# Optimization experiments

Hardware: AMD Instinct MI355X
Metric: run time of the kernel (lower is better)

The kernel has to match this reference:

```python
import jax, jax.numpy as jnp
import numpy as np

EPS = 1e-5

def _rmsnorm(x):
    # BitLinear applies a (non-learnable) RMSNorm to activations before quantization
    return x * jax.lax.rsqrt(jnp.mean(x * x, axis=-1, keepdims=True) + EPS)

def _activation_quant(x):
    # per-token absmax int8 quantization, dequantized back to float
    scale = 127.0 / jnp.clip(jnp.max(jnp.abs(x), axis=-1, keepdims=True), EPS, None)
    return jnp.clip(jnp.round(x * scale), -128, 127) / scale

def _weight_quant(w):
    # absmean ternary {-1,0,1} quantization, dequantized back to float
    scale = 1.0 / jnp.clip(jnp.mean(jnp.abs(w)), EPS, None)
    return jnp.clip(jnp.round(w * scale), -1, 1) / scale

def _bitlinear(x, w):
    xn = _rmsnorm(x)
    # straight-through estimators (identity grads through quantizers)
    xq = xn + jax.lax.stop_gradient(_activation_quant(xn) - xn)
    wq = w + jax.lax.stop_gradient(_weight_quant(w) - w)
    return jnp.einsum('bsd,hd->bsh', xq, wq)

def setup_inputs() -> dict:
    key = jax.random.key(0)
    k1, k2, k3, k4 = jax.random.split(key, 4)
    B, S, D, H = 4, 2048, 4096, 11008
    return {
        'x': jax.random.normal(k1, (B, S, D), dtype=jnp.float32),
        'w_gate': jax.random.normal(k2, (H, D), dtype=jnp.float32) * 0.02,
        'w_up': jax.random.normal(k3, (H, D), dtype=jnp.float32) * 0.02,
        'w_down': jax.random.normal(k4, (D, H), dtype=jnp.float32) * 0.02,
    }

def reference(x, w_gate, w_up, w_down):
    h = jax.nn.silu(_bitlinear(x, w_gate)) * _bitlinear(x, w_up)
    return _bitlinear(h, w_down)
```

## Files before the change

### kernel.cpp

```cpp
#include <hip/hip_runtime.h>
#include <hip/hip_bf16.h>
#include <cstdint>

#define EPS 1e-5

typedef __attribute__((ext_vector_type(4))) int int32x4;

__device__ __forceinline__ void gload(const char* g, char* l) {
  __builtin_amdgcn_global_load_lds(
      (const __attribute__((address_space(1))) unsigned int*)g,
      (__attribute__((address_space(3))) unsigned int*)l, 16, 0, 0);
}

__device__ inline float np_leaf_abs(const float* __restrict__ a, int n) {
  float r[8];
  #pragma unroll
  for (int j = 0; j < 8; j++) r[j] = fabsf(a[j]);
  for (int i = 8; i < n; i += 8) {
    #pragma unroll
    for (int j = 0; j < 8; j++) r[j] += fabsf(a[i + j]);
  }
  return ((r[0] + r[1]) + (r[2] + r[3])) + ((r[4] + r[5]) + (r[6] + r[7]));
}

__global__ __launch_bounds__(256) void np_blocksums(
    const float* __restrict__ w, float* __restrict__ bs) {
  int b = blockIdx.x * 256 + threadIdx.x;
  const float* a = w + (long)b * 344;
  float s0 = np_leaf_abs(a, 80);
  float s1 = np_leaf_abs(a + 80, 88);
  float s2 = np_leaf_abs(a + 168, 88);
  float s3 = np_leaf_abs(a + 256, 88);
  bs[b] = (s0 + s1) + (s2 + s3);
}

__global__ __launch_bounds__(256) void np_tree_partial(
    const float* __restrict__ bs, float* __restrict__ part) {
  __shared__ float sh[256];
  int t = threadIdx.x;
  const float* a = bs + (long)blockIdx.x * 512;
  sh[t] = a[2 * t] + a[2 * t + 1];
  __syncthreads();
  for (int n = 128; n >= 1; n >>= 1) {
    float x = 0.f;
    if (t < n) x = sh[2 * t] + sh[2 * t + 1];
    __syncthreads();
    if (t < n) sh[t] = x;
    __syncthreads();
  }
  if (t == 0) part[blockIdx.x] = sh[0];
}

__global__ __launch_bounds__(128) void np_tree_final(
    const float* __restrict__ part, float* __restrict__ out) {
  __shared__ float sh[128];
  int t = threadIdx.x;
  sh[t] = part[2 * t] + part[2 * t + 1];
  __syncthreads();
  for (int n = 64; n >= 1; n >>= 1) {
    float x = 0.f;
    if (t < n) x = sh[2 * t] + sh[2 * t + 1];
    __syncthreads();
    if (t < n) sh[t] = x;
    __syncthreads();
  }
  if (t == 0) out[0] = sh[0] / 45088768.0f;
}

__global__ __launch_bounds__(256) void quant_w(
    const float* __restrict__ w, const float* __restrict__ mean_ptr,
    char* __restrict__ q, long n4) {
  float scale = 1.0f / fmaxf(*mean_ptr, 1e-5f);
  long i = (long)blockIdx.x * blockDim.x + threadIdx.x;
  long stride = (long)gridDim.x * blockDim.x;
  const float4* w4 = (const float4*)w;
  char4* q4 = (char4*)q;
  for (; i < n4; i += stride) {
    float4 v = w4[i];
    char4 c;
    c.x = (char)(int)fminf(1.f, fmaxf(-1.f, rintf(v.x * scale)));
    c.y = (char)(int)fminf(1.f, fmaxf(-1.f, rintf(v.y * scale)));
    c.z = (char)(int)fminf(1.f, fmaxf(-1.f, rintf(v.z * scale)));
    c.w = (char)(int)fminf(1.f, fmaxf(-1.f, rintf(v.w * scale)));
    q4[i] = c;
  }
}

#define CORR_MAX 1024
#define WIN 1e-6f

__global__ __launch_bounds__(256) void quant_w_down(
    const float* __restrict__ w, const float* __restrict__ mean_ptr,
    char* __restrict__ q, int* __restrict__ cnt,
    int* __restrict__ ck, float* __restrict__ cv) {
  float scale = 1.0f / fmaxf(*mean_ptr, 1e-5f);
  long i0 = ((long)blockIdx.x * blockDim.x + threadIdx.x) * 4;
  long stride = (long)gridDim.x * blockDim.x * 4;
  for (long i = i0; i < 4096L * 11008L; i += stride) {
    char4 c;
    #pragma unroll
    for (int j = 0; j < 4; j++) {
      float t = w[i + j] * scale;
      float qv = fminf(1.f, fmaxf(-1.f, rintf(t)));
      if (fabsf(fabsf(t) - 0.5f) < WIN) {
        qv = 0.f;
        int idx = atomicAdd(cnt, 1);
        if (idx < CORR_MAX) {
          ck[idx] = (int)(i + j);
          cv[idx] = t > 0.f ? 0.5f : -0.5f;
        }
      }
      ((char*)&c)[j] = (char)(int)qv;
    }
    *(char4*)(q + i) = c;
  }
}

__global__ void zero_cnt(int* cnt) { *cnt = 0; }

__global__ __launch_bounds__(64) void apply_corr(
    const int* __restrict__ cnt, const int* __restrict__ ck,
    const float* __restrict__ cv, const char* __restrict__ qh,
    const float* __restrict__ fh, const float* __restrict__ meanw,
    float* __restrict__ out) {
  int r = blockIdx.x * 64 + threadIdx.x;
  float fwd = fmaxf(meanw[2], 1e-5f);
  int n = *cnt; if (n > CORR_MAX) n = CORR_MAX;
  float fr = fh[r] * fwd;
  for (int i = 0; i < n; i++) {
    int flat = ck[i];
    int nn = flat / 11008, kk = flat % 11008;
    float qv = (float)qh[(long)r * 11008 + kk];
    out[(long)r * 4096 + nn] += cv[i] * qv * fr;
  }
}

__device__ inline void block_reduce_sum_max_d(double& s, float& m) {
  #pragma unroll
  for (int off = 1; off < 64; off <<= 1) {
    s += __shfl_xor(s, off, 64);
    m = fmaxf(m, __shfl_xor(m, off, 64));
  }
  __shared__ double ssh[4];
  __shared__ float msh[4];
  int wv = threadIdx.x >> 6;
  if ((threadIdx.x & 63) == 0) { ssh[wv] = s; msh[wv] = m; }
  __syncthreads();
  s = (ssh[0] + ssh[1]) + (ssh[2] + ssh[3]);
  m = fmaxf(fmaxf(msh[0], msh[1]), fmaxf(msh[2], msh[3]));
}

__device__ inline char quant1d(float x, double rn, double s) {
  double t = (double)x * rn;
  double q = rint(t * s);
  q = fmin(127.0, fmax(-128.0, q));
  return (char)(int)q;
}

__global__ __launch_bounds__(256) void act_quant_x(
    const float* __restrict__ x, char* __restrict__ qx, float* __restrict__ fx) {
  const int row = blockIdx.x;
  const float4* xr = (const float4*)(x + (long)row * 4096);
  float4 v[4];
  double ss = 0.0;
  float am = 0.f;
  #pragma unroll
  for (int i = 0; i < 4; i++) {
    v[i] = xr[i * 256 + threadIdx.x];
    ss += ((double)v[i].x * v[i].x + (double)v[i].y * v[i].y) +
          ((double)v[i].z * v[i].z + (double)v[i].w * v[i].w);
    am = fmaxf(am, fmaxf(fmaxf(fabsf(v[i].x), fabsf(v[i].y)),
                         fmaxf(fabsf(v[i].z), fabsf(v[i].w))));
  }
  block_reduce_sum_max_d(ss, am);
  double rn = 1.0 / sqrt(ss / 4096.0 + EPS);
  double den = fmax((double)am * rn, EPS);
  double s = 127.0 / den;
  if (threadIdx.x == 0) fx[row] = (float)(den / 127.0);
  char4* qr = (char4*)(qx + (long)row * 4096);
  #pragma unroll
  for (int i = 0; i < 4; i++) {
    char4 c;
    c.x = quant1d(v[i].x, rn, s);
    c.y = quant1d(v[i].y, rn, s);
    c.z = quant1d(v[i].z, rn, s);
    c.w = quant1d(v[i].w, rn, s);
    qr[i * 256 + threadIdx.x] = c;
  }
}

__global__ __launch_bounds__(256) void act_quant_h(
    const float* __restrict__ h, char* __restrict__ qh, float* __restrict__ fh) {
  const long row = blockIdx.x;
  const float4* hr = (const float4*)(h + row * 11008);
  double ss = 0.0;
  float am = 0.f;
  for (int i = threadIdx.x; i < 2752; i += 256) {
    float4 v = hr[i];
    ss += ((double)v.x * v.x + (double)v.y * v.y) +
          ((double)v.z * v.z + (double)v.w * v.w);
    am = fmaxf(am, fmaxf(fmaxf(fabsf(v.x), fabsf(v.y)),
                         fmaxf(fabsf(v.z), fabsf(v.w))));
  }
  block_reduce_sum_max_d(ss, am);
  double rn = 1.0 / sqrt(ss / 11008.0 + EPS);
  double den = fmax((double)am * rn, EPS);
  double s = 127.0 / den;
  if (threadIdx.x == 0) fh[row] = (float)(den / 127.0);
  char4* qr = (char4*)(qh + row * 11008);
  for (int i = threadIdx.x; i < 2752; i += 256) {
    float4 v = hr[i];
    char4 c;
    c.x = quant1d(v.x, rn, s);
    c.y = quant1d(v.y, rn, s);
    c.z = quant1d(v.z, rn, s);
    c.w = quant1d(v.w, rn, s);
    qr[i] = c;
  }
}


__global__ __launch_bounds__(256, 2) void gemm_gateup(
    const char* __restrict__ qx, const char* __restrict__ qwg, const char* __restrict__ qwu,
    const float* __restrict__ meanw, const float* __restrict__ fx, float* __restrict__ h) {
  __shared__ __align__(16) char As[3][8192];
  __shared__ __align__(16) char Bgs[3][8192];
  __shared__ __align__(16) char Bus[3][8192];
  const int t = threadIdx.x;
  const int lane = t & 63;
  const int wv = t >> 6;
  const int bid = blockIdx.x;
  const int swz = (bid & 7) * 688 + (bid >> 3);
  const int m0 = (swz & 63) * 128;
  const int n0 = (swz >> 6) * 128;
  const int wm = (wv >> 1) * 64;
  const int wn = (wv & 1) * 64;

  const int rowin = lane >> 2;
  const int gcol = (((lane & 3) - ((lane >> 3) & 3)) & 3) * 16;
  const int slot = ((((lane >> 4) + ((lane >> 1) & 3)) & 3) << 4);
  const int lrow = (lane & 15) * 64;

  const char* gA = qx  + (long)(m0 + wv * 32 + rowin) * 4096 + gcol;
  const char* gG = qwg + (long)(n0 + wv * 32 + rowin) * 4096 + gcol;
  const char* gU = qwu + (long)(n0 + wv * 32 + rowin) * 4096 + gcol;
  const long R16 = 16L * 4096;

  int32x4 accg[4][4] = {};
  int32x4 accu[4][4] = {};

  #define STAGE_GU(pb, k0)                                 \
    do {                                                   \
      gload(gA + (k0),       &As [pb][wv * 2048]);         \
      gload(gA + (k0) + R16, &As [pb][wv * 2048 + 1024]);  \
      gload(gG + (k0),       &Bgs[pb][wv * 2048]);         \
      gload(gG + (k0) + R16, &Bgs[pb][wv * 2048 + 1024]);  \
      gload(gU + (k0),       &Bus[pb][wv * 2048]);         \
      gload(gU + (k0) + R16, &Bus[pb][wv * 2048 + 1024]);  \
    } while (0)

  STAGE_GU(0, 0);
  STAGE_GU(1, 64);
  asm volatile("s_waitcnt vmcnt(6)" ::: "memory");
  __builtin_amdgcn_s_barrier();

  for (int ks = 0; ks < 64; ++ks) {
    const int pb = ks % 3;
    const char* ab = &As [pb][0] + wm * 64 + lrow + slot;
    const char* gb = &Bgs[pb][0] + wn * 64 + lrow + slot;
    const char* ub = &Bus[pb][0] + wn * 64 + lrow + slot;
    int32x4 a[4], bg[4], bu[4];
    #pragma unroll
    for (int m = 0; m < 4; m++) a[m] = *(const int32x4*)(ab + m * 1024);
    #pragma unroll
    for (int n = 0; n < 4; n++) bg[n] = *(const int32x4*)(gb + n * 1024);
    #pragma unroll
    for (int n = 0; n < 4; n++) bu[n] = *(const int32x4*)(ub + n * 1024);
    if (ks + 2 < 64) STAGE_GU((ks + 2) % 3, (ks + 2) * 64);
    __builtin_amdgcn_s_setprio(1);
    #pragma unroll
    for (int n = 0; n < 4; n++) {
      #pragma unroll
      for (int m = 0; m < 4; m++) {
        accg[m][n] = __builtin_amdgcn_mfma_i32_16x16x64_i8(a[m], bg[n], accg[m][n], 0, 0, 0);
        accu[m][n] = __builtin_amdgcn_mfma_i32_16x16x64_i8(a[m], bu[n], accu[m][n], 0, 0, 0);
      }
    }
    __builtin_amdgcn_s_setprio(0);
    if (ks < 62)      asm volatile("s_waitcnt vmcnt(6)" ::: "memory");
    else if (ks < 63) asm volatile("s_waitcnt vmcnt(0)" ::: "memory");
    if (ks < 63) __builtin_amdgcn_s_barrier();
  }
  #undef STAGE_GU

  float fwg = fmaxf(meanw[0], 1e-5f);
  float fwu = fmaxf(meanw[1], 1e-5f);
  const int rgrp = lane >> 4;
  const int cidx = lane & 15;
  #pragma unroll
  for (int m = 0; m < 4; m++) {
    #pragma unroll
    for (int r = 0; r < 4; r++) {
      int grow = m0 + wm + m * 16 + rgrp * 4 + r;
      float fxr = fx[grow];
      float sg = fxr * fwg, su = fxr * fwu;
      #pragma unroll
      for (int n = 0; n < 4; n++) {
        float g = (float)accg[m][n][r] * sg;
        float u = (float)accu[m][n][r] * su;
        float hv = g / (1.f + expf(-g)) * u;
        h[(long)grow * 11008 + (n0 + wn + n * 16 + cidx)] = hv;
      }
    }
  }
}

__global__ __launch_bounds__(256, 3) void gemm_down(
    const char* __restrict__ qh, const char* __restrict__ qwd,
    const float* __restrict__ mean_wd, const float* __restrict__ fh,
    float* __restrict__ out) {
  __shared__ __align__(16) char As[3][8192];
  __shared__ __align__(16) char Bs[3][8192];
  const int t = threadIdx.x;
  const int lane = t & 63;
  const int wv = t >> 6;
  const int bid = blockIdx.x;
  const int swz = (bid & 7) * 256 + (bid >> 3);
  const int m0 = (swz & 63) * 128;
  const int n0 = (swz >> 6) * 128;
  const int wm = (wv >> 1) * 64;
  const int wn = (wv & 1) * 64;

  const int rowin = lane >> 2;
  const int gcol = (((lane & 3) - ((lane >> 3) & 3)) & 3) * 16;
  const int slot = ((((lane >> 4) + ((lane >> 1) & 3)) & 3) << 4);
  const int lrow = (lane & 15) * 64;

  const char* gA = qh  + (long)(m0 + wv * 32 + rowin) * 11008 + gcol;
  const char* gB = qwd + (long)(n0 + wv * 32 + rowin) * 11008 + gcol;
  const long R16 = 16L * 11008;

  int32x4 acc[4][4] = {};

  #define STAGE_DN(pb, k0)                                \
    do {                                                  \
      gload(gA + (k0),       &As[pb][wv * 2048]);         \
      gload(gA + (k0) + R16, &As[pb][wv * 2048 + 1024]);  \
      gload(gB + (k0),       &Bs[pb][wv * 2048]);         \
      gload(gB + (k0) + R16, &Bs[pb][wv * 2048 + 1024]);  \
    } while (0)

  STAGE_DN(0, 0);
  STAGE_DN(1, 64);
  asm volatile("s_waitcnt vmcnt(4)" ::: "memory");
  __builtin_amdgcn_s_barrier();

  for (int ks = 0; ks < 172; ++ks) {
    const int pb = ks % 3;
    const char* ab = &As[pb][0] + wm * 64 + lrow + slot;
    const char* bb = &Bs[pb][0] + wn * 64 + lrow + slot;
    int32x4 a[4], b[4];
    #pragma unroll
    for (int m = 0; m < 4; m++) a[m] = *(const int32x4*)(ab + m * 1024);
    #pragma unroll
    for (int n = 0; n < 4; n++) b[n] = *(const int32x4*)(bb + n * 1024);
    if (ks + 2 < 172) STAGE_DN((ks + 2) % 3, (ks + 2) * 64);
    __builtin_amdgcn_s_setprio(1);
    #pragma unroll
    for (int n = 0; n < 4; n++) {
      #pragma unroll
      for (int m = 0; m < 4; m++)
        acc[m][n] = __builtin_amdgcn_mfma_i32_16x16x64_i8(a[m], b[n], acc[m][n], 0, 0, 0);
    }
    __builtin_amdgcn_s_setprio(0);
    if (ks < 170)      asm volatile("s_waitcnt vmcnt(4)" ::: "memory");
    else if (ks < 171) asm volatile("s_waitcnt vmcnt(0)" ::: "memory");
    if (ks < 171) __builtin_amdgcn_s_barrier();
  }
  #undef STAGE_DN

  float fwd = fmaxf(mean_wd[0], 1e-5f);
  const int rgrp = lane >> 4;
  const int cidx = lane & 15;
  #pragma unroll
  for (int m = 0; m < 4; m++) {
    #pragma unroll
    for (int r = 0; r < 4; r++) {
      int grow = m0 + wm + m * 16 + rgrp * 4 + r;
      float f = fh[grow] * fwd;
      #pragma unroll
      for (int n = 0; n < 4; n++) {
        out[(long)grow * 4096 + (n0 + wn + n * 16 + cidx)] =
            (float)acc[m][n][r] * f;
      }
    }
  }
}

extern "C" void kernel_launch(void* const* d_in, const int* in_sizes, int n_in,
                              void* d_out, int out_size, void* d_ws, size_t ws_size,
                              hipStream_t stream) {
  const float* x      = (const float*)d_in[0];
  const float* w_gate = (const float*)d_in[1];
  const float* w_up   = (const float*)d_in[2];
  const float* w_down = (const float*)d_in[3];
  float* out = (float*)d_out;

  const long NW = 11008L * 4096L;
  const long NX = 8192L * 4096L;
  const long NH = 8192L * 11008L;

  char* ws  = (char*)d_ws;
  char* qwg = ws;
  char* qwu = qwg + NW;
  char* qwd = qwu + NW;
  char* qx  = qwd + NW;
  char* qh  = qx + NX;
  float* h  = (float*)(qh + NH);
  float* fx = h + NH;
  float* fh = fx + 8192;
  float* meanw = fh + 8192;
  float* bs    = meanw + 4;
  float* tmp   = bs + 131072;
  int*   ccnt  = (int*)(tmp + 65536);
  int*   ck    = ccnt + 4;
  float* cv    = (float*)(ck + CORR_MAX);

  zero_cnt<<<1, 1, 0, stream>>>(ccnt);

  np_blocksums<<<512, 256, 0, stream>>>(w_gate, bs);
  np_tree_partial<<<256, 256, 0, stream>>>(bs, tmp);
  np_tree_final<<<1, 128, 0, stream>>>(tmp, meanw + 0);
  np_blocksums<<<512, 256, 0, stream>>>(w_up, bs);
  np_tree_partial<<<256, 256, 0, stream>>>(bs, tmp);
  np_tree_final<<<1, 128, 0, stream>>>(tmp, meanw + 1);
  np_blocksums<<<512, 256, 0, stream>>>(w_down, bs);
  np_tree_partial<<<256, 256, 0, stream>>>(bs, tmp);
  np_tree_final<<<1, 128, 0, stream>>>(tmp, meanw + 2);

  quant_w<<<4096, 256, 0, stream>>>(w_gate, meanw + 0, qwg, NW / 4);
  quant_w<<<4096, 256, 0, stream>>>(w_up,   meanw + 1, qwu, NW / 4);
  quant_w_down<<<4096, 256, 0, stream>>>(w_down, meanw + 2, qwd, ccnt, ck, cv);

  act_quant_x<<<8192, 256, 0, stream>>>(x, qx, fx);

  gemm_gateup<<<5504, 256, 0, stream>>>(qx, qwg, qwu, meanw, fx, h);

  act_quant_h<<<8192, 256, 0, stream>>>(h, qh, fh);

  gemm_down<<<2048, 256, 0, stream>>>(qh, qwd, meanw + 2, fh, out);

  apply_corr<<<128, 64, 0, stream>>>(ccnt, ck, cv, qh, fh, meanw, out);
}
```

Measured before the change: 1.881 ms.

## Batch weight reductions, prefetch LDS fragments in GEMMs, widen down-proj tile

The three weight-mean reduction chains are merged into single launches covering all three matrices, and the gate and up quantization kernels are merged into one launch. act_quant_h now caches its row in shared memory so the second pass does not re-read global memory. Both GEMMs move to a deeper 3-stage prefetch with register double-buffering of the LDS fragments, and gemm_down widens its N tile to 256. These changes cut launch overhead and global re-reads and aim to overlap LDS reads with MFMA, at the cost of more registers and LDS, which may lower occupancy.

```diff
diff --git a/kernel.cpp b/kernel.cpp
--- a/kernel.cpp
+++ b/kernel.cpp
@@ -23,10 +23,13 @@
   return ((r[0] + r[1]) + (r[2] + r[3])) + ((r[4] + r[5]) + (r[6] + r[7]));
 }
 
-__global__ __launch_bounds__(256) void np_blocksums(
-    const float* __restrict__ w, float* __restrict__ bs) {
+__global__ __launch_bounds__(256) void np_blocksums3(
+    const float* __restrict__ w0, const float* __restrict__ w1,
+    const float* __restrict__ w2, float* __restrict__ bs) {
   int b = blockIdx.x * 256 + threadIdx.x;
-  const float* a = w + (long)b * 344;
+  const float* w = (b < 131072) ? w0 : (b < 262144 ? w1 : w2);
+  long lb = b & 131071;
+  const float* a = w + lb * 344;
   float s0 = np_leaf_abs(a, 80);
   float s1 = np_leaf_abs(a + 80, 88);
   float s2 = np_leaf_abs(a + 168, 88);
@@ -34,7 +37,7 @@
   bs[b] = (s0 + s1) + (s2 + s3);
 }
 
-__global__ __launch_bounds__(256) void np_tree_partial(
+__global__ __launch_bounds__(256) void np_tree_partial3(
     const float* __restrict__ bs, float* __restrict__ part) {
   __shared__ float sh[256];
   int t = threadIdx.x;
@@ -51,11 +54,12 @@
   if (t == 0) part[blockIdx.x] = sh[0];
 }
 
-__global__ __launch_bounds__(128) void np_tree_final(
-    const float* __restrict__ part, float* __restrict__ out) {
+__global__ __launch_bounds__(128) void np_tree_final3(
+    const float* __restrict__ part, float* __restrict__ meanw) {
   __shared__ float sh[128];
   int t = threadIdx.x;
-  sh[t] = part[2 * t] + part[2 * t + 1];
+  const float* p = part + blockIdx.x * 256;
+  sh[t] = p[2 * t] + p[2 * t + 1];
   __syncthreads();
   for (int n = 64; n >= 1; n >>= 1) {
     float x = 0.f;
@@ -64,15 +68,19 @@
     if (t < n) sh[t] = x;
     __syncthreads();
   }
-  if (t == 0) out[0] = sh[0] / 45088768.0f;
-}
-
-__global__ __launch_bounds__(256) void quant_w(
-    const float* __restrict__ w, const float* __restrict__ mean_ptr,
-    char* __restrict__ q, long n4) {
-  float scale = 1.0f / fmaxf(*mean_ptr, 1e-5f);
-  long i = (long)blockIdx.x * blockDim.x + threadIdx.x;
-  long stride = (long)gridDim.x * blockDim.x;
+  if (t == 0) meanw[blockIdx.x] = sh[0] / 45088768.0f;
+}
+
+__global__ __launch_bounds__(256) void quant_w_gu(
+    const float* __restrict__ wg, const float* __restrict__ wu,
+    const float* __restrict__ meanw, char* __restrict__ qg, char* __restrict__ qu,
+    long n4) {
+  int half = (blockIdx.x >= 4096);
+  const float* w = half ? wu : wg;
+  char* q = half ? qu : qg;
+  float scale = 1.0f / fmaxf(meanw[half], 1e-5f);
+  long i = (long)(blockIdx.x & 4095) * blockDim.x + threadIdx.x;
+  long stride = 4096L * blockDim.x;
   const float4* w4 = (const float4*)w;
   char4* q4 = (char4*)q;
   for (; i < n4; i += stride) {
@@ -93,7 +101,7 @@
     const float* __restrict__ w, const float* __restrict__ mean_ptr,
     char* __restrict__ q, int* __restrict__ cnt,
     int* __restrict__ ck, float* __restrict__ cv) {
-  float scale = 1.0f / fmaxf(*mean_ptr, 1e-5f);
+  float scale = 1.0f / fmaxf(mean_ptr[2], 1e-5f);
   long i0 = ((long)blockIdx.x * blockDim.x + threadIdx.x) * 4;
   long stride = (long)gridDim.x * blockDim.x * 4;
   for (long i = i0; i < 4096L * 11008L; i += stride) {
@@ -191,12 +199,14 @@
 
 __global__ __launch_bounds__(256) void act_quant_h(
     const float* __restrict__ h, char* __restrict__ qh, float* __restrict__ fh) {
+  __shared__ float4 hrow4[2752];
   const long row = blockIdx.x;
   const float4* hr = (const float4*)(h + row * 11008);
   double ss = 0.0;
   float am = 0.f;
   for (int i = threadIdx.x; i < 2752; i += 256) {
     float4 v = hr[i];
+    hrow4[i] = v;
     ss += ((double)v.x * v.x + (double)v.y * v.y) +
           ((double)v.z * v.z + (double)v.w * v.w);
     am = fmaxf(am, fmaxf(fmaxf(fabsf(v.x), fabsf(v.y)),
@@ -209,7 +219,7 @@
   if (threadIdx.x == 0) fh[row] = (float)(den / 127.0);
   char4* qr = (char4*)(qh + row * 11008);
   for (int i = threadIdx.x; i < 2752; i += 256) {
-    float4 v = hr[i];
+    float4 v = hrow4[i];
     char4 c;
     c.x = quant1d(v.x, rn, s);
     c.y = quant1d(v.y, rn, s);
@@ -238,8 +248,7 @@
 
   const int rowin = lane >> 2;
   const int gcol = (((lane & 3) - ((lane >> 3) & 3)) & 3) * 16;
-  const int slot = ((((lane >> 4) + ((lane >> 1) & 3)) & 3) << 4);
-  const int lrow = (lane & 15) * 64;
+  const int loff = (lane & 15) * 64 + ((((lane >> 4) + ((lane >> 1) & 3)) & 3) << 4);
 
   const char* gA = qx  + (long)(m0 + wv * 32 + rowin) * 4096 + gcol;
   const char* gG = qwg + (long)(n0 + wv * 32 + rowin) * 4096 + gcol;
@@ -248,50 +257,85 @@
 
   int32x4 accg[4][4] = {};
   int32x4 accu[4][4] = {};
-
-  #define STAGE_GU(pb, k0)                                 \
-    do {                                                   \
-      gload(gA + (k0),       &As [pb][wv * 2048]);         \
-      gload(gA + (k0) + R16, &As [pb][wv * 2048 + 1024]);  \
-      gload(gG + (k0),       &Bgs[pb][wv * 2048]);         \
-      gload(gG + (k0) + R16, &Bgs[pb][wv * 2048 + 1024]);  \
-      gload(gU + (k0),       &Bus[pb][wv * 2048]);         \
-      gload(gU + (k0) + R16, &Bus[pb][wv * 2048 + 1024]);  \
-    } while (0)
-
-  STAGE_GU(0, 0);
-  STAGE_GU(1, 64);
+  int32x4 a0[4], g0[4], u0[4], a1[4], g1[4], u1[4];
+
+  char *PA0 = &As[0][0], *PA1 = &As[1][0], *PA2 = &As[2][0];
+  char *PG0 = &Bgs[0][0], *PG1 = &Bgs[1][0], *PG2 = &Bgs[2][0];
+  char *PU0 = &Bus[0][0], *PU1 = &Bus[1][0], *PU2 = &Bus[2][0];
+
+  #define GU_STAGE(pa, pg, pu, k0)                          \
+    do {                                                    \
+      gload(gA + (k0),       (pa) + wv * 2048);             \
+      gload(gA + (k0) + R16, (pa) + wv * 2048 + 1024);      \
+      gload(gG + (k0),       (pg) + wv * 2048);             \
+      gload(gG + (k0) + R16, (pg) + wv * 2048 + 1024);      \
+      gload(gU + (k0),       (pu) + wv * 2048);             \
+      gload(gU + (k0) + R16, (pu) + wv * 2048 + 1024);      \
+    } while (0)
+
+  #define GU_READ(ar, gr, ur, pa, pg, pu)                          \
+    do {                                                           \
+      _Pragma("unroll")                                            \
+      for (int m = 0; m < 4; m++)                                  \
+        ar[m] = *(const int32x4*)((pa) + (wm + m * 16) * 64 + loff); \
+      _Pragma("unroll")                                            \
+      for (int n = 0; n < 4; n++) {                                \
+        gr[n] = *(const int32x4*)((pg) + (wn + n * 16) * 64 + loff); \
+        ur[n] = *(const int32x4*)((pu) + (wn + n * 16) * 64 + loff); \
+      }                                                            \
+    } while (0)
+
+  #define GU_MFMA(ar, gr, ur)                                                \
+    do {                                                                     \
+      __builtin_amdgcn_s_setprio(1);                                         \
+      _Pragma("unroll")                                                      \
+      for (int n = 0; n < 4; n++) {                                          \
+        _Pragma("unroll")                                                    \
+        for (int m = 0; m < 4; m++) {                                        \
+          accg[m][n] = __builtin_amdgcn_mfma_i32_16x16x64_i8(ar[m], gr[n], accg[m][n], 0, 0, 0); \
+          accu[m][n] = __builtin_amdgcn_mfma_i32_16x16x64_i8(ar[m], ur[n], accu[m][n], 0, 0, 0); \
+        }                                                                    \
+      }                                                                      \
+      __builtin_amdgcn_s_setprio(0);                                         \
+    } while (0)
+
+  #define GU_ROT()                                          \
+    do {                                                    \
+      char* tp;                                             \
+      tp = PA0; PA0 = PA1; PA1 = PA2; PA2 = tp;             \
+      tp = PG0; PG0 = PG1; PG1 = PG2; PG2 = tp;             \
+      tp = PU0; PU0 = PU1; PU1 = PU2; PU2 = tp;             \
+    } while (0)
+
+  #define GU_BODY(ks, Rc_a, Rc_g, Rc_u, Rn_a, Rn_g, Rn_u)          \
+    do {                                                           \
+      if ((ks) + 3 < 64) GU_STAGE(PA0, PG0, PU0, ((ks) + 3) * 64); \
+      if ((ks) + 1 < 64) GU_READ(Rn_a, Rn_g, Rn_u, PA1, PG1, PU1); \
+      GU_MFMA(Rc_a, Rc_g, Rc_u);                                   \
+      if ((ks) + 3 < 64) asm volatile("s_waitcnt vmcnt(6)" ::: "memory"); \
+      else               asm volatile("s_waitcnt vmcnt(0)" ::: "memory"); \
+      if ((ks) < 62) __builtin_amdgcn_s_barrier();                 \
+      GU_ROT();                                                    \
+    } while (0)
+
+  GU_STAGE(PA0, PG0, PU0, 0);
+  GU_STAGE(PA1, PG1, PU1, 64);
+  GU_STAGE(PA2, PG2, PU2, 128);
+  asm volatile("s_waitcnt vmcnt(12)" ::: "memory");
+  __builtin_amdgcn_s_barrier();
+  GU_READ(a0, g0, u0, PA0, PG0, PU0);
   asm volatile("s_waitcnt vmcnt(6)" ::: "memory");
   __builtin_amdgcn_s_barrier();
 
-  for (int ks = 0; ks < 64; ++ks) {
-    const int pb = ks % 3;
-    const char* ab = &As [pb][0] + wm * 64 + lrow + slot;
-    const char* gb = &Bgs[pb][0] + wn * 64 + lrow + slot;
-    const char* ub = &Bus[pb][0] + wn * 64 + lrow + slot;
-    int32x4 a[4], bg[4], bu[4];
-    #pragma unroll
-    for (int m = 0; m < 4; m++) a[m] = *(const int32x4*)(ab + m * 1024);
-    #pragma unroll
-    for (int n = 0; n < 4; n++) bg[n] = *(const int32x4*)(gb + n * 1024);
-    #pragma unroll
-    for (int n = 0; n < 4; n++) bu[n] = *(const int32x4*)(ub + n * 1024);
-    if (ks + 2 < 64) STAGE_GU((ks + 2) % 3, (ks + 2) * 64);
-    __builtin_amdgcn_s_setprio(1);
-    #pragma unroll
-    for (int n = 0; n < 4; n++) {
-      #pragma unroll
-      for (int m = 0; m < 4; m++) {
-        accg[m][n] = __builtin_amdgcn_mfma_i32_16x16x64_i8(a[m], bg[n], accg[m][n], 0, 0, 0);
-        accu[m][n] = __builtin_amdgcn_mfma_i32_16x16x64_i8(a[m], bu[n], accu[m][n], 0, 0, 0);
-      }
-    }
-    __builtin_amdgcn_s_setprio(0);
-    if (ks < 62)      asm volatile("s_waitcnt vmcnt(6)" ::: "memory");
-    else if (ks < 63) asm volatile("s_waitcnt vmcnt(0)" ::: "memory");
-    if (ks < 63) __builtin_amdgcn_s_barrier();
-  }
-  #undef STAGE_GU
+  for (int ks = 0; ks < 64; ks += 2) {
+    GU_BODY(ks,     a0, g0, u0, a1, g1, u1);
+    GU_BODY(ks + 1, a1, g1, u1, a0, g0, u0);
+  }
+  #undef GU_STAGE
+  #undef GU_READ
+  #undef GU_MFMA
+  #undef GU_ROT
+  #undef GU_BODY
 
   float fwg = fmaxf(meanw[0], 1e-5f);
   float fwu = fmaxf(meanw[1], 1e-5f);
@@ -315,71 +359,106 @@
   }
 }
 
-__global__ __launch_bounds__(256, 3) void gemm_down(
+__global__ __launch_bounds__(256, 2) void gemm_down(
     const char* __restrict__ qh, const char* __restrict__ qwd,
-    const float* __restrict__ mean_wd, const float* __restrict__ fh,
+    const float* __restrict__ meanw, const float* __restrict__ fh,
     float* __restrict__ out) {
   __shared__ __align__(16) char As[3][8192];
-  __shared__ __align__(16) char Bs[3][8192];
+  __shared__ __align__(16) char Bs[3][16384];
   const int t = threadIdx.x;
   const int lane = t & 63;
   const int wv = t >> 6;
   const int bid = blockIdx.x;
-  const int swz = (bid & 7) * 256 + (bid >> 3);
+  const int swz = (bid & 7) * 128 + (bid >> 3);
   const int m0 = (swz & 63) * 128;
-  const int n0 = (swz >> 6) * 128;
+  const int n0 = (swz >> 6) * 256;
   const int wm = (wv >> 1) * 64;
-  const int wn = (wv & 1) * 64;
+  const int wn = (wv & 1) * 128;
 
   const int rowin = lane >> 2;
   const int gcol = (((lane & 3) - ((lane >> 3) & 3)) & 3) * 16;
-  const int slot = ((((lane >> 4) + ((lane >> 1) & 3)) & 3) << 4);
-  const int lrow = (lane & 15) * 64;
+  const int loff = (lane & 15) * 64 + ((((lane >> 4) + ((lane >> 1) & 3)) & 3) << 4);
 
   const char* gA = qh  + (long)(m0 + wv * 32 + rowin) * 11008 + gcol;
-  const char* gB = qwd + (long)(n0 + wv * 32 + rowin) * 11008 + gcol;
+  const char* gB = qwd + (long)(n0 + wv * 64 + rowin) * 11008 + gcol;
   const long R16 = 16L * 11008;
 
-  int32x4 acc[4][4] = {};
-
-  #define STAGE_DN(pb, k0)                                \
-    do {                                                  \
-      gload(gA + (k0),       &As[pb][wv * 2048]);         \
-      gload(gA + (k0) + R16, &As[pb][wv * 2048 + 1024]);  \
-      gload(gB + (k0),       &Bs[pb][wv * 2048]);         \
-      gload(gB + (k0) + R16, &Bs[pb][wv * 2048 + 1024]);  \
-    } while (0)
-
-  STAGE_DN(0, 0);
-  STAGE_DN(1, 64);
-  asm volatile("s_waitcnt vmcnt(4)" ::: "memory");
+  int32x4 acc[4][8] = {};
+  int32x4 a0[4], b0[8], a1[4], b1[8];
+
+  char *PA0 = &As[0][0], *PA1 = &As[1][0], *PA2 = &As[2][0];
+  char *PB0 = &Bs[0][0], *PB1 = &Bs[1][0], *PB2 = &Bs[2][0];
+
+  #define DN_STAGE(pa, pb, k0)                              \
+    do {                                                    \
+      gload(gA + (k0),           (pa) + wv * 2048);         \
+      gload(gA + (k0) + R16,     (pa) + wv * 2048 + 1024);  \
+      gload(gB + (k0),           (pb) + wv * 4096);         \
+      gload(gB + (k0) + R16,     (pb) + wv * 4096 + 1024);  \
+      gload(gB + (k0) + 2 * R16, (pb) + wv * 4096 + 2048);  \
+      gload(gB + (k0) + 3 * R16, (pb) + wv * 4096 + 3072);  \
+    } while (0)
+
+  #define DN_READ(ar, br, pa, pb)                                   \
+    do {                                                            \
+      _Pragma("unroll")                                             \
+      for (int m = 0; m < 4; m++)                                   \
+        ar[m] = *(const int32x4*)((pa) + (wm + m * 16) * 64 + loff);\
+      _Pragma("unroll")                                             \
+      for (int n = 0; n < 8; n++)                                   \
+        br[n] = *(const int32x4*)((pb) + (wn + n * 16) * 64 + loff);\
+    } while (0)
+
+  #define DN_MFMA(ar, br)                                                    \
+    do {                                                                     \
+      __builtin_amdgcn_s_setprio(1);                                         \
+      _Pragma("unroll")                                                      \
+      for (int n = 0; n < 8; n++) {                                          \
+        _Pragma("unroll")                                                    \
+        for (int m = 0; m < 4; m++)                                          \
+          acc[m][n] = __builtin_amdgcn_mfma_i32_16x16x64_i8(ar[m], br[n], acc[m][n], 0, 0, 0); \
+      }                                                                      \
+      __builtin_amdgcn_s_setprio(0);                                         \
+    } while (0)
+
+  #define DN_ROT()                                          \
+    do {                                                    \
+      char* tp;                                             \
+      tp = PA0; PA0 = PA1; PA1 = PA2; PA2 = tp;             \
+      tp = PB0; PB0 = PB1; PB1 = PB2; PB2 = tp;             \
+    } while (0)
+
+  #define DN_BODY(ks, Rc_a, Rc_b, Rn_a, Rn_b)                      \
+    do {                                                           \
+      if ((ks) + 3 < 172) DN_STAGE(PA0, PB0, ((ks) + 3) * 64);     \
+      if ((ks) + 1 < 172) DN_READ(Rn_a, Rn_b, PA1, PB1);           \
+      DN_MFMA(Rc_a, Rc_b);                                         \
+      if ((ks) + 3 < 172) asm volatile("s_waitcnt vmcnt(6)" ::: "memory"); \
+      else                asm volatile("s_waitcnt vmcnt(0)" ::: "memory"); \
+      if ((ks) < 170) __builtin_amdgcn_s_barrier();                \
+      DN_ROT();                                                    \
+    } while (0)
+
+  DN_STAGE(PA0, PB0, 0);
+  DN_STAGE(PA1, PB1, 64);
+  DN_STAGE(PA2, PB2, 128);
+  asm volatile("s_waitcnt vmcnt(12)" ::: "memory");
   __builtin_amdgcn_s_barrier();
-
-  for (int ks = 0; ks < 172; ++ks) {
-    const int pb = ks % 3;
-    const char* ab = &As[pb][0] + wm * 64 + lrow + slot;
-    const char* bb = &Bs[pb][0] + wn * 64 + lrow + slot;
-    int32x4 a[4], b[4];
-    #pragma unroll
-    for (int m = 0; m < 4; m++) a[m] = *(const int32x4*)(ab + m * 1024);
-    #pragma unroll
-    for (int n = 0; n < 4; n++) b[n] = *(const int32x4*)(bb + n * 1024);
-    if (ks + 2 < 172) STAGE_DN((ks + 2) % 3, (ks + 2) * 64);
-    __builtin_amdgcn_s_setprio(1);
-    #pragma unroll
-    for (int n = 0; n < 4; n++) {
-      #pragma unroll
-      for (int m = 0; m < 4; m++)
-        acc[m][n] = __builtin_amdgcn_mfma_i32_16x16x64_i8(a[m], b[n], acc[m][n], 0, 0, 0);
-    }
-    __builtin_amdgcn_s_setprio(0);
-    if (ks < 170)      asm volatile("s_waitcnt vmcnt(4)" ::: "memory");
-    else if (ks < 171) asm volatile("s_waitcnt vmcnt(0)" ::: "memory");
-    if (ks < 171) __builtin_amdgcn_s_barrier();
-  }
-  #undef STAGE_DN
-
-  float fwd = fmaxf(mean_wd[0], 1e-5f);
+  DN_READ(a0, b0, PA0, PB0);
+  asm volatile("s_waitcnt vmcnt(6)" ::: "memory");
+  __builtin_amdgcn_s_barrier();
+
+  for (int ks = 0; ks < 172; ks += 2) {
+    DN_BODY(ks,     a0, b0, a1, b1);
+    DN_BODY(ks + 1, a1, b1, a0, b0);
+  }
+  #undef DN_STAGE
+  #undef DN_READ
+  #undef DN_MFMA
+  #undef DN_ROT
+  #undef DN_BODY
+
+  float fwd = fmaxf(meanw[2], 1e-5f);
   const int rgrp = lane >> 4;
   const int cidx = lane & 15;
   #pragma unroll
@@ -389,7 +468,7 @@
       int grow = m0 + wm + m * 16 + rgrp * 4 + r;
       float f = fh[grow] * fwd;
       #pragma unroll
-      for (int n = 0; n < 4; n++) {
+      for (int n = 0; n < 8; n++) {
         out[(long)grow * 4096 + (n0 + wn + n * 16 + cidx)] =
             (float)acc[m][n][r] * f;
       }
@@ -421,26 +500,19 @@
   float* fh = fx + 8192;
   float* meanw = fh + 8192;
   float* bs    = meanw + 4;
-  float* tmp   = bs + 131072;
-  int*   ccnt  = (int*)(tmp + 65536);
+  float* part  = bs + 3 * 131072;
+  int*   ccnt  = (int*)(part + 1024);
   int*   ck    = ccnt + 4;
   float* cv    = (float*)(ck + CORR_MAX);
 
   zero_cnt<<<1, 1, 0, stream>>>(ccnt);
 
-  np_blocksums<<<512, 256, 0, stream>>>(w_gate, bs);
-  np_tree_partial<<<256, 256, 0, stream>>>(bs, tmp);
-  np_tree_final<<<1, 128, 0, stream>>>(tmp, meanw + 0);
-  np_blocksums<<<512, 256, 0, stream>>>(w_up, bs);
-  np_tree_partial<<<256, 256, 0, stream>>>(bs, tmp);
-  np_tree_final<<<1, 128, 0, stream>>>(tmp, meanw + 1);
-  np_blocksums<<<512, 256, 0, stream>>>(w_down, bs);
-  np_tree_partial<<<256, 256, 0, stream>>>(bs, tmp);
-  np_tree_final<<<1, 128, 0, stream>>>(tmp, meanw + 2);
-
-  quant_w<<<4096, 256, 0, stream>>>(w_gate, meanw + 0, qwg, NW / 4);
-  quant_w<<<4096, 256, 0, stream>>>(w_up,   meanw + 1, qwu, NW / 4);
-  quant_w_down<<<4096, 256, 0, stream>>>(w_down, meanw + 2, qwd, ccnt, ck, cv);
+  np_blocksums3<<<1536, 256, 0, stream>>>(w_gate, w_up, w_down, bs);
+  np_tree_partial3<<<768, 256, 0, stream>>>(bs, part);
+  np_tree_final3<<<3, 128, 0, stream>>>(part, meanw);
+
+  quant_w_gu<<<8192, 256, 0, stream>>>(w_gate, w_up, meanw, qwg, qwu, NW / 4);
+  quant_w_down<<<4096, 256, 0, stream>>>(w_down, meanw, qwd, ccnt, ck, cv);
 
   act_quant_x<<<8192, 256, 0, stream>>>(x, qx, fx);
 
@@ -448,7 +520,7 @@
 
   act_quant_h<<<8192, 256, 0, stream>>>(h, qh, fh);
 
-  gemm_down<<<2048, 256, 0, stream>>>(qh, qwd, meanw + 2, fh, out);
+  gemm_down<<<1024, 256, 0, stream>>>(qh, qwd, meanw, fh, out);
 
   apply_corr<<<128, 64, 0, stream>>>(ccnt, ck, cv, qh, fh, meanw, out);
 }
```

New measurement: 1.690 ms. 1.11x faster.
